# Kernel tuning notes

Measured on AMD Instinct MI355X. Metric: run time of the kernel, lower is better.

The kernel has to match this reference:

```python
import jax, jax.numpy as jnp
import numpy as np

D_MODEL = 1024
HID = 4096  # d_model * att_size
N_KEYS = 65536
TOP_K = 6


def setup_inputs() -> dict:
    root = jax.random.key(0)
    k0, k1, k2, k3, k4, k5 = jax.random.split(root, 6)
    s = 1.0 / np.sqrt(D_MODEL)
    return {
        "query": jax.random.normal(k0, (D_MODEL,), dtype=jnp.float32),
        "key_mat": jax.random.normal(k1, (N_KEYS, D_MODEL), dtype=jnp.float32),
        "Wq": jax.random.normal(k2, (HID, D_MODEL), dtype=jnp.float32) * s,
        "bq": jax.random.normal(k3, (HID,), dtype=jnp.float32) * s,
        "Wk": jax.random.normal(k4, (HID, D_MODEL), dtype=jnp.float32) * s,
        "bk": jax.random.normal(k5, (HID,), dtype=jnp.float32) * s,
    }


def reference(query, key_mat, Wq, bq, Wk, bk):
    # Linear projections (nn.Linear: x @ W^T + b)
    q = jnp.dot(Wq, query) + bq                 # [HID]
    k = jnp.dot(key_mat, Wk.T) + bk             # [N, HID]
    scores = jnp.dot(k, q)                      # [N]
    # The torch loop does k=6 sequential argmax + mask(-100000) + gather,
    # which (absent pathological -100000 scores) is exactly top-6 selection.
    _, idx = jax.lax.top_k(scores, TOP_K)       # [TOP_K]
    return jnp.mean(key_mat[idx], axis=0)       # [D_MODEL]
```

## Files before the change

### kernel.cpp

```cpp
#include <hip/hip_runtime.h>

#define DM    1024
#define HID   4096
#define NKEYS 65536
#define TOPK  6

__global__ __launch_bounds__(256) void qproj_kernel(const float* __restrict__ Wq,
                                                    const float* __restrict__ query,
                                                    const float* __restrict__ bq,
                                                    float* __restrict__ q) {
    const int wave = threadIdx.x >> 6;
    const int lane = threadIdx.x & 63;
    const int h = blockIdx.x * 4 + wave;
    const float4* __restrict__ Wrow = (const float4*)(Wq + (size_t)h * DM);
    const float4* __restrict__ qv   = (const float4*)query;
    float acc = 0.f;
#pragma unroll
    for (int k = 0; k < 4; ++k) {
        float4 w = Wrow[lane + k * 64];
        float4 x = qv[lane + k * 64];
        acc += w.x * x.x + w.y * x.y + w.z * x.z + w.w * x.w;
    }
#pragma unroll
    for (int off = 32; off > 0; off >>= 1) acc += __shfl_down(acc, off);
    if (lane == 0) q[h] = acc + bq[h];
}

__global__ __launch_bounds__(256) void vproj_kernel(const float* __restrict__ Wk,
                                                    const float* __restrict__ q,
                                                    float* __restrict__ v_part) {
    const int t  = threadIdx.x;
    const int b  = blockIdx.x;
    const int h0 = b * 16;
    float4 acc = {0.f, 0.f, 0.f, 0.f};
#pragma unroll 4
    for (int j = 0; j < 16; ++j) {
        const int h = h0 + j;
        const float qh = q[h];
        float4 w = ((const float4*)(Wk + (size_t)h * DM))[t];
        acc.x += w.x * qh; acc.y += w.y * qh; acc.z += w.z * qh; acc.w += w.w * qh;
    }
    ((float4*)(v_part + (size_t)b * DM))[t] = acc;
}

__global__ __launch_bounds__(256) void vreduce_kernel(const float* __restrict__ v_part,
                                                      float* __restrict__ v) {
    const int d = blockIdx.x * 256 + threadIdx.x;
    float acc = 0.f;
    for (int b = 0; b < 256; ++b) acc += v_part[(size_t)b * DM + d];
    v[d] = acc;
}

__global__ __launch_bounds__(256) void score_kernel(const float* __restrict__ key_mat,
                                                    const float* __restrict__ v,
                                                    float* __restrict__ scores) {
    const int wave = threadIdx.x >> 6;
    const int lane = threadIdx.x & 63;
    const int r = blockIdx.x * 4 + wave;
    const float4* __restrict__ row = (const float4*)(key_mat + (size_t)r * DM);
    const float4* __restrict__ vv  = (const float4*)v;
    float acc = 0.f;
#pragma unroll
    for (int k = 0; k < 4; ++k) {
        float4 a = row[lane + k * 64];
        float4 b = vv[lane + k * 64];
        acc += a.x * b.x + a.y * b.y + a.z * b.z + a.w * b.w;
    }
#pragma unroll
    for (int off = 32; off > 0; off >>= 1) acc += __shfl_down(acc, off);
    if (lane == 0) scores[r] = acc;
}

__global__ __launch_bounds__(1024) void topk_mean_kernel(const float* __restrict__ scores,
                                                         const float* __restrict__ key_mat,
                                                         float* __restrict__ out) {
    const int t = threadIdx.x;
    const float NEG = -3.4e38f;

    float bv[TOPK]; int bi[TOPK];
#pragma unroll
    for (int j = 0; j < TOPK; ++j) { bv[j] = NEG; bi[j] = 0; }
    for (int j = 0; j < 64; ++j) {
        const int i = j * 1024 + t;
        const float s = scores[i];
        if (s > bv[TOPK - 1]) {
            int p = TOPK - 1;
            while (p > 0 && bv[p - 1] < s) { bv[p] = bv[p - 1]; bi[p] = bi[p - 1]; --p; }
            bv[p] = s; bi[p] = i;
        }
    }

    __shared__ float cv[1024 * TOPK];
    __shared__ int   ci[1024 * TOPK];
    __shared__ float rv[1024];
    __shared__ int   rp[1024];
    __shared__ int   sel[TOPK];
#pragma unroll
    for (int j = 0; j < TOPK; ++j) { cv[t * TOPK + j] = bv[j]; ci[t * TOPK + j] = bi[j]; }
    __syncthreads();

    for (int p = 0; p < TOPK; ++p) {
        float m = NEG; int mp = 0;
#pragma unroll
        for (int j = 0; j < TOPK; ++j) {
            const float val = cv[t * TOPK + j];
            if (val > m) { m = val; mp = t * TOPK + j; }
        }
        rv[t] = m; rp[t] = mp;
        __syncthreads();
        for (int s = 512; s > 0; s >>= 1) {
            if (t < s) {
                if (rv[t + s] > rv[t]) { rv[t] = rv[t + s]; rp[t] = rp[t + s]; }
            }
            __syncthreads();
        }
        if (t == 0) { sel[p] = ci[rp[0]]; cv[rp[0]] = NEG; }
        __syncthreads();
    }

    float acc = 0.f;
#pragma unroll
    for (int p = 0; p < TOPK; ++p) acc += key_mat[(size_t)sel[p] * DM + t];
    out[t] = acc * (1.0f / 6.0f);
}

extern "C" void kernel_launch(void* const* d_in, const int* in_sizes, int n_in,
                              void* d_out, int out_size, void* d_ws, size_t ws_size,
                              hipStream_t stream) {
    const float* query   = (const float*)d_in[0];
    const float* key_mat = (const float*)d_in[1];
    const float* Wq      = (const float*)d_in[2];
    const float* bq      = (const float*)d_in[3];
    const float* Wk      = (const float*)d_in[4];
    float* out = (float*)d_out;

    float* ws      = (float*)d_ws;
    float* q       = ws;
    float* v_part  = q + HID;
    float* v       = v_part + 256 * DM;
    float* scores  = v + DM;

    qproj_kernel  <<<HID / 4, 256, 0, stream>>>(Wq, query, bq, q);
    vproj_kernel  <<<256,     256, 0, stream>>>(Wk, q, v_part);
    vreduce_kernel<<<DM / 256,256, 0, stream>>>(v_part, v);
    score_kernel  <<<NKEYS/4, 256, 0, stream>>>(key_mat, v, scores);
    topk_mean_kernel<<<1,    1024, 0, stream>>>(scores, key_mat, out);
}
```

Before: 440.2 us.

## Split top-k into parallel per-block stage and small merge; use nontemporal loads

Replaces the single-block top-k over all 65536 scores with a two-stage scheme: 256 blocks each extract their local top-6 through wave-shuffle argmax, then one block merges the 1536 candidates and averages the selected rows. This removes the serial single-workgroup scan, which was a long tail. Streaming loads of Wq, Wk and key_mat now use nontemporal hints, and vreduce runs with 64-thread blocks so more blocks share the work. In exchange it adds one kernel launch and a small workspace for the candidates.

```diff
diff --git a/kernel.cpp b/kernel.cpp
--- a/kernel.cpp
+++ b/kernel.cpp
@@ -4,6 +4,13 @@
 #define HID   4096
 #define NKEYS 65536
 #define TOPK  6
+#define NEGF  (-3.4e38f)
+
+typedef float fvec4 __attribute__((ext_vector_type(4)));
+
+__device__ __forceinline__ fvec4 nt_load4(const float* p) {
+    return __builtin_nontemporal_load((const fvec4*)p);
+}
 
 __global__ __launch_bounds__(256) void qproj_kernel(const float* __restrict__ Wq,
                                                     const float* __restrict__ query,
@@ -12,13 +19,13 @@
     const int wave = threadIdx.x >> 6;
     const int lane = threadIdx.x & 63;
     const int h = blockIdx.x * 4 + wave;
-    const float4* __restrict__ Wrow = (const float4*)(Wq + (size_t)h * DM);
-    const float4* __restrict__ qv   = (const float4*)query;
+    const float* Wrow = Wq + (size_t)h * DM;
+    const fvec4* __restrict__ qv = (const fvec4*)query;
     float acc = 0.f;
 #pragma unroll
     for (int k = 0; k < 4; ++k) {
-        float4 w = Wrow[lane + k * 64];
-        float4 x = qv[lane + k * 64];
+        fvec4 w = nt_load4(Wrow + (lane + k * 64) * 4);
+        fvec4 x = qv[lane + k * 64];
         acc += w.x * x.x + w.y * x.y + w.z * x.z + w.w * x.w;
     }
 #pragma unroll
@@ -32,21 +39,22 @@
     const int t  = threadIdx.x;
     const int b  = blockIdx.x;
     const int h0 = b * 16;
-    float4 acc = {0.f, 0.f, 0.f, 0.f};
+    fvec4 acc = {0.f, 0.f, 0.f, 0.f};
 #pragma unroll 4
     for (int j = 0; j < 16; ++j) {
         const int h = h0 + j;
         const float qh = q[h];
-        float4 w = ((const float4*)(Wk + (size_t)h * DM))[t];
-        acc.x += w.x * qh; acc.y += w.y * qh; acc.z += w.z * qh; acc.w += w.w * qh;
+        fvec4 w = nt_load4(Wk + (size_t)h * DM + t * 4);
+        acc += w * qh;
     }
-    ((float4*)(v_part + (size_t)b * DM))[t] = acc;
+    *(fvec4*)(v_part + (size_t)b * DM + t * 4) = acc;
 }
 
-__global__ __launch_bounds__(256) void vreduce_kernel(const float* __restrict__ v_part,
-                                                      float* __restrict__ v) {
-    const int d = blockIdx.x * 256 + threadIdx.x;
+__global__ __launch_bounds__(64) void vreduce_kernel(const float* __restrict__ v_part,
+                                                     float* __restrict__ v) {
+    const int d = blockIdx.x * 64 + threadIdx.x;
     float acc = 0.f;
+#pragma unroll 8
     for (int b = 0; b < 256; ++b) acc += v_part[(size_t)b * DM + d];
     v[d] = acc;
 }
@@ -57,13 +65,13 @@
     const int wave = threadIdx.x >> 6;
     const int lane = threadIdx.x & 63;
     const int r = blockIdx.x * 4 + wave;
-    const float4* __restrict__ row = (const float4*)(key_mat + (size_t)r * DM);
-    const float4* __restrict__ vv  = (const float4*)v;
+    const float* row = key_mat + (size_t)r * DM;
+    const fvec4* __restrict__ vv = (const fvec4*)v;
     float acc = 0.f;
 #pragma unroll
     for (int k = 0; k < 4; ++k) {
-        float4 a = row[lane + k * 64];
-        float4 b = vv[lane + k * 64];
+        fvec4 a = nt_load4(row + (lane + k * 64) * 4);
+        fvec4 b = vv[lane + k * 64];
         acc += a.x * b.x + a.y * b.y + a.z * b.z + a.w * b.w;
     }
 #pragma unroll
@@ -71,57 +79,96 @@
     if (lane == 0) scores[r] = acc;
 }
 
-__global__ __launch_bounds__(1024) void topk_mean_kernel(const float* __restrict__ scores,
-                                                         const float* __restrict__ key_mat,
-                                                         float* __restrict__ out) {
+__global__ __launch_bounds__(256) void topk_stage1(const float* __restrict__ scores,
+                                                   float* __restrict__ cand_v,
+                                                   int* __restrict__ cand_i) {
+    const int t = threadIdx.x, b = blockIdx.x;
+    const int i = b * 256 + t;
+    float cur = scores[i];
+
+    __shared__ float wv[4];
+    __shared__ int   wi[4];
+    __shared__ float selv[TOPK];
+    __shared__ int   seli[TOPK];
+
+    for (int p = 0; p < TOPK; ++p) {
+        float m = cur; int mi = i;
+#pragma unroll
+        for (int off = 32; off > 0; off >>= 1) {
+            float ov = __shfl_down(m, off);
+            int   oi = __shfl_down(mi, off);
+            if (ov > m) { m = ov; mi = oi; }
+        }
+        const int lane = t & 63, w = t >> 6;
+        if (lane == 0) { wv[w] = m; wi[w] = mi; }
+        __syncthreads();
+        if (t == 0) {
+            float bm = wv[0]; int bix = wi[0];
+#pragma unroll
+            for (int j = 1; j < 4; ++j) if (wv[j] > bm) { bm = wv[j]; bix = wi[j]; }
+            selv[p] = bm; seli[p] = bix;
+        }
+        __syncthreads();
+        if (i == seli[p]) cur = NEGF;
+    }
+    if (t < TOPK) { cand_v[b * TOPK + t] = selv[t]; cand_i[b * TOPK + t] = seli[t]; }
+}
+
+__global__ __launch_bounds__(256) void topk_stage2_mean(const float* __restrict__ cand_v,
+                                                        const int* __restrict__ cand_i,
+                                                        const float* __restrict__ key_mat,
+                                                        float* __restrict__ out) {
     const int t = threadIdx.x;
-    const float NEG = -3.4e38f;
+    const int NC = 256 * TOPK;
 
-    float bv[TOPK]; int bi[TOPK];
+    __shared__ float sv[NC];
+    __shared__ int   si[NC];
+    __shared__ float wv[4];
+    __shared__ int   wi[4];
+    __shared__ int   sel[TOPK];
+
 #pragma unroll
-    for (int j = 0; j < TOPK; ++j) { bv[j] = NEG; bi[j] = 0; }
-    for (int j = 0; j < 64; ++j) {
-        const int i = j * 1024 + t;
-        const float s = scores[i];
-        if (s > bv[TOPK - 1]) {
-            int p = TOPK - 1;
-            while (p > 0 && bv[p - 1] < s) { bv[p] = bv[p - 1]; bi[p] = bi[p - 1]; --p; }
-            bv[p] = s; bi[p] = i;
-        }
+    for (int j = 0; j < TOPK; ++j) {
+        sv[t + j * 256] = cand_v[t + j * 256];
+        si[t + j * 256] = cand_i[t + j * 256];
     }
-
-    __shared__ float cv[1024 * TOPK];
-    __shared__ int   ci[1024 * TOPK];
-    __shared__ float rv[1024];
-    __shared__ int   rp[1024];
-    __shared__ int   sel[TOPK];
-#pragma unroll
-    for (int j = 0; j < TOPK; ++j) { cv[t * TOPK + j] = bv[j]; ci[t * TOPK + j] = bi[j]; }
     __syncthreads();
 
     for (int p = 0; p < TOPK; ++p) {
-        float m = NEG; int mp = 0;
+        float m = NEGF; int mp = 0;
 #pragma unroll
         for (int j = 0; j < TOPK; ++j) {
-            const float val = cv[t * TOPK + j];
-            if (val > m) { m = val; mp = t * TOPK + j; }
+            const int pos = t * TOPK + j;
+            const float val = sv[pos];
+            if (val > m) { m = val; mp = pos; }
         }
-        rv[t] = m; rp[t] = mp;
+#pragma unroll
+        for (int off = 32; off > 0; off >>= 1) {
+            float ov = __shfl_down(m, off);
+            int   op = __shfl_down(mp, off);
+            if (ov > m) { m = ov; mp = op; }
+        }
+        const int lane = t & 63, w = t >> 6;
+        if (lane == 0) { wv[w] = m; wi[w] = mp; }
         __syncthreads();
-        for (int s = 512; s > 0; s >>= 1) {
-            if (t < s) {
-                if (rv[t + s] > rv[t]) { rv[t] = rv[t + s]; rp[t] = rp[t + s]; }
-            }
-            __syncthreads();
+        if (t == 0) {
+            float bm = wv[0]; int bp = wi[0];
+#pragma unroll
+            for (int j = 1; j < 4; ++j) if (wv[j] > bm) { bm = wv[j]; bp = wi[j]; }
+            sel[p] = si[bp];
+            sv[bp] = NEGF;
         }
-        if (t == 0) { sel[p] = ci[rp[0]]; cv[rp[0]] = NEG; }
         __syncthreads();
     }
 
-    float acc = 0.f;
+    fvec4 acc = {0.f, 0.f, 0.f, 0.f};
 #pragma unroll
-    for (int p = 0; p < TOPK; ++p) acc += key_mat[(size_t)sel[p] * DM + t];
-    out[t] = acc * (1.0f / 6.0f);
+    for (int p = 0; p < TOPK; ++p) {
+        fvec4 r = *(const fvec4*)(key_mat + (size_t)sel[p] * DM + t * 4);
+        acc += r;
+    }
+    acc *= (1.0f / 6.0f);
+    *(fvec4*)(out + t * 4) = acc;
 }
 
 extern "C" void kernel_launch(void* const* d_in, const int* in_sizes, int n_in,
@@ -139,10 +186,13 @@
     float* v_part  = q + HID;
     float* v       = v_part + 256 * DM;
     float* scores  = v + DM;
+    float* cand_v  = scores + NKEYS;
+    int*   cand_i  = (int*)(cand_v + 256 * TOPK);
 
-    qproj_kernel  <<<HID / 4, 256, 0, stream>>>(Wq, query, bq, q);
-    vproj_kernel  <<<256,     256, 0, stream>>>(Wk, q, v_part);
-    vreduce_kernel<<<DM / 256,256, 0, stream>>>(v_part, v);
-    score_kernel  <<<NKEYS/4, 256, 0, stream>>>(key_mat, v, scores);
-    topk_mean_kernel<<<1,    1024, 0, stream>>>(scores, key_mat, out);
+    qproj_kernel     <<<HID / 4,  256, 0, stream>>>(Wq, query, bq, q);
+    vproj_kernel     <<<256,      256, 0, stream>>>(Wk, q, v_part);
+    vreduce_kernel   <<<DM / 64,  64,  0, stream>>>(v_part, v);
+    score_kernel     <<<NKEYS / 4,256, 0, stream>>>(key_mat, v, scores);
+    topk_stage1      <<<256,      256, 0, stream>>>(scores, cand_v, cand_i);
+    topk_stage2_mean <<<1,        256, 0, stream>>>(cand_v, cand_i, key_mat, out);
 }
```

Result: faster. 383.2 us (-13.0%).
